# Performance work log

Hardware: AMD Instinct MI355X
Metric: run time of the kernel (lower is better)

The kernel has to match this reference:

```python
import jax, jax.numpy as jnp
import numpy as np


def gcn_conv(x, edge_index, W, b):
    """PyG-style GCNConv: add self-loops, symmetric D^-1/2 (A+I) D^-1/2 norm,
    linear transform before propagation, bias after aggregation."""
    N = x.shape[0]
    src, dst = edge_index[0], edge_index[1]
    loops = jnp.arange(N, dtype=edge_index.dtype)
    src_a = jnp.concatenate([src, loops])  # [E+N]
    dst_a = jnp.concatenate([dst, loops])
    deg = jax.ops.segment_sum(jnp.ones_like(src_a, dtype=x.dtype), dst_a, num_segments=N)
    inv_sqrt = jnp.where(deg > 0, jax.lax.rsqrt(deg), 0.0)
    norm = inv_sqrt[src_a] * inv_sqrt[dst_a]  # [E+N]
    h = x @ W  # [N, out]
    out = jax.ops.segment_sum(h[src_a] * norm[:, None], dst_a, num_segments=N)
    return out + b


def gcn_branch(x, edge_index, W1, b1, W2, b2):
    h = jax.nn.relu(gcn_conv(x, edge_index, W1, b1))
    h = jax.nn.relu(gcn_conv(h, edge_index, W2, b2))
    # global_add_pool with batch = zeros -> sum over all nodes, shape [1, h2]
    return jnp.sum(h, axis=0, keepdims=True)


def setup_inputs() -> dict:
    key = jax.random.key(0)
    ks = jax.random.split(key, 12)
    Nm, Em = 50000, 800000
    Np, Ep = 100000, 1600000
    h1, h2 = 128, 128
    fc_in = 2 * h2 + 1
    inp = {
        "mol_x": jax.random.normal(ks[0], (Nm, 1), jnp.float32),
        "mol_edge_index": jax.random.randint(ks[1], (2, Em), 0, Nm, jnp.int64),
        "prot_x": jax.random.normal(ks[2], (Np, 1), jnp.float32),
        "prot_edge_index": jax.random.randint(ks[3], (2, Ep), 0, Np, jnp.int64),
        "phys_energy": jax.random.normal(ks[4], (1,), jnp.float32),
        "W1": jax.random.normal(ks[5], (1, h1), jnp.float32) / np.sqrt(1.0),
        "b1": jnp.zeros((h1,), jnp.float32),
        "W2": jax.random.normal(ks[6], (h1, h2), jnp.float32) / np.sqrt(h1),
        "b2": jnp.zeros((h2,), jnp.float32),
        "Wfc": jax.random.normal(ks[7], (fc_in, 1), jnp.float32) / np.sqrt(fc_in),
        "bfc": jnp.zeros((1,), jnp.float32),
    }
    return inp


def reference(mol_x, mol_edge_index, prot_x, prot_edge_index, phys_energy,
              W1, b1, W2, b2, Wfc, bfc):
    x1 = gcn_branch(mol_x, mol_edge_index, W1, b1, W2, b2)    # [1, h2]
    x2 = gcn_branch(prot_x, prot_edge_index, W1, b1, W2, b2)  # [1, h2]
    combined = jnp.concatenate([x1, x2, phys_energy.reshape(1, -1)], axis=-1)
    return combined @ Wfc + bfc  # [1, 1]
```

## Files before the change

### kernel.cpp

```cpp
#include <hip/hip_runtime.h>

#define CDIV(a,b) (((a)+(b)-1)/(b))
#define BINCAP 4096


__global__ __launch_bounds__(256) void k_count(
        const int* __restrict__ me, const int* __restrict__ pe,
        int Em, int Ep, int Nm, int per, int NBKT, int* __restrict__ btot,
        const float* __restrict__ b1, const float* __restrict__ W1,
        const float* __restrict__ W2, float* __restrict__ u, float* __restrict__ v,
        int* __restrict__ flags) {
    __shared__ int cnt[64];
    __shared__ int nz;
    int t = threadIdx.x, blk = blockIdx.x;
    int Etot = Em + Ep;
    int e0 = blk * per, e1 = min(e0 + per, Etot);
    if (t < 64) cnt[t] = 0;
    __syncthreads();
    for (int e = e0 + t; e < e1; e += 256) {
        int d = (e < Em) ? me[Em + e] : (pe[Ep + (e - Em)] + Nm);
        atomicAdd(&cnt[d >> 12], 1);
    }
    __syncthreads();
    if (t < NBKT && cnt[t]) atomicAdd(&btot[t], cnt[t]);
    if (blk == 0) {
        if (t == 0) nz = 0;
        __syncthreads();
        if (t < 128) {
            if (b1[t] != 0.f) atomicOr(&nz, 1);
            float au = 0.f, av = 0.f;
            for (int j = 0; j < 128; ++j) {
                float w = W1[j], w2 = W2[j * 128 + t];
                au = fmaf(fmaxf(w, 0.f), w2, au);
                av = fmaf(fmaxf(-w, 0.f), w2, av);
            }
            u[t] = au; v[t] = av;
        }
        __syncthreads();
        if (t == 0) flags[0] = nz;
    }
}

__global__ __launch_bounds__(256) void k_bin(
        const int* __restrict__ me, const int* __restrict__ pe,
        int Em, int Ep, int Nm, int per, int NBKT,
        const int* __restrict__ btot, int* __restrict__ gcur, int* __restrict__ pkb) {
    __shared__ int lpk[BINCAP];
    __shared__ unsigned char lbkt[BINCAP];
    __shared__ int cnt[64], cst[64], cur[64], wbase[64], bb[64];
    int t = threadIdx.x;
    int Etot = Em + Ep;
    int e0 = blockIdx.x * per, e1 = min(e0 + per, Etot);
    int ne = max(e1 - e0, 0);
    if (t < 64) cnt[t] = 0;
    __syncthreads();
    for (int e = e0 + t; e < e1; e += 256) {
        int d = (e < Em) ? me[Em + e] : (pe[Ep + (e - Em)] + Nm);
        atomicAdd(&cnt[d >> 12], 1);
    }
    __syncthreads();
    if (t == 0) {
        int run = 0, runb = 0;
        for (int b = 0; b < NBKT; ++b) {
            cst[b] = run; cur[b] = run; run += cnt[b];
            bb[b] = runb; runb += btot[b];
        }
    }
    __syncthreads();
    if (t < NBKT) wbase[t] = bb[t] + (cnt[t] ? atomicAdd(&gcur[t], cnt[t]) : 0);
    __syncthreads();
    for (int e = e0 + t; e < e1; e += 256) {
        int s, d;
        if (e < Em) { s = me[e];            d = me[Em + e]; }
        else        { int ee = e - Em; s = pe[ee] + Nm; d = pe[Ep + ee] + Nm; }
        int b = d >> 12;
        int p = atomicAdd(&cur[b], 1);
        lpk[p]  = ((d & 4095) << 18) | s;
        lbkt[p] = (unsigned char)b;
    }
    __syncthreads();
    for (int i = t; i < ne; i += 256) {
        int b = lbkt[i];
        pkb[wbase[b] + (i - cst[b])] = lpk[i];
    }
}

__global__ __launch_bounds__(256) void k_accA(
        const int* __restrict__ pkb, const int* __restrict__ btot,
        int NBKT, int WPB, int Ntot, int* __restrict__ hist) {
    __shared__ int h[4096];
    __shared__ int sbs, sbe;
    int b = blockIdx.x / WPB, sl = blockIdx.x % WPB, t = threadIdx.x;
    if (t == 0) {
        int run = 0;
        for (int i = 0; i < b; ++i) run += btot[i];
        sbs = run; sbe = run + btot[b];
    }
    for (int k = t; k < 4096; k += 256) h[k] = 0;
    __syncthreads();
    for (int i = sbs + sl * 256 + t; i < sbe; i += WPB * 256)
        atomicAdd(&h[pkb[i] >> 18], 1);
    __syncthreads();
    for (int k = t; k < 4096; k += 256) {
        int vv = h[k];
        int node = (b << 12) + k;
        if (vv && node < Ntot) atomicAdd(&hist[node], vv);
    }
}

__global__ void k_inv(const int* __restrict__ hist,
                      const float* __restrict__ mx, const float* __restrict__ px,
                      int Nm, int Ntot, float* __restrict__ xi) {
    int g = blockIdx.x * 256 + threadIdx.x;
    if (g < Ntot) {
        float x = (g < Nm) ? mx[g] : px[g - Nm];
        xi[g] = x * rsqrtf((float)(hist[g] + 1));
    }
}

__global__ __launch_bounds__(256) void k_accB(
        const int* __restrict__ pkb, const int* __restrict__ btot,
        const float* __restrict__ xi, int NBKT, int WPB, int Ntot,
        float* __restrict__ s_acc) {
    __shared__ float acc[4096];
    __shared__ int sbs, sbe;
    int b = blockIdx.x / WPB, sl = blockIdx.x % WPB, t = threadIdx.x;
    if (t == 0) {
        int run = 0;
        for (int i = 0; i < b; ++i) run += btot[i];
        sbs = run; sbe = run + btot[b];
    }
    for (int k = t; k < 4096; k += 256) acc[k] = 0.f;
    __syncthreads();
    for (int i = sbs + sl * 256 + t; i < sbe; i += WPB * 256) {
        int pk = pkb[i];
        atomicAdd(&acc[pk >> 18], xi[pk & 0x3FFFF]);
    }
    __syncthreads();
    for (int k = t; k < 4096; k += 256) {
        float vv = acc[k];
        int node = (b << 12) + k;
        if (vv != 0.f && node < Ntot) atomicAdd(&s_acc[node], vv);
    }
}

__global__ void k_s(const int* __restrict__ hist, const float* __restrict__ s_acc,
                    const float* __restrict__ xi, int Ntot, float2* __restrict__ si) {
    int i = blockIdx.x * 256 + threadIdx.x;
    if (i >= Ntot) return;
    float iv = rsqrtf((float)(hist[i] + 1));
    si[i] = make_float2(iv * (s_acc[i] + xi[i]), iv);
}

__global__ __launch_bounds__(256) void k_accC(
        const int* __restrict__ pkb, const int* __restrict__ btot,
        const float2* __restrict__ si, int NBKT, int WPB, int Ntot,
        float* __restrict__ PM, const int* __restrict__ flags) {
    if (flags[0]) return;
    __shared__ float pm[8192];
    __shared__ int sbs, sbe;
    int b = blockIdx.x / WPB, sl = blockIdx.x % WPB, t = threadIdx.x;
    if (t == 0) {
        int run = 0;
        for (int i = 0; i < b; ++i) run += btot[i];
        sbs = run; sbe = run + btot[b];
    }
    for (int k = t; k < 8192; k += 256) pm[k] = 0.f;
    __syncthreads();
    for (int i = sbs + sl * 256 + t; i < sbe; i += WPB * 256) {
        int pk = pkb[i];
        float2 q = si[pk & 0x3FFFF];
        float val = q.y * q.x;
        int lo = (pk >> 18) * 2;
        if (val > 0.f)      atomicAdd(&pm[lo],     val);
        else if (val < 0.f) atomicAdd(&pm[lo + 1], -val);
    }
    __syncthreads();
    for (int k = t; k < 8192; k += 256) {
        float vv = pm[k];
        int node = (b << 12) + (k >> 1);
        if (vv != 0.f && node < Ntot) atomicAdd(&PM[2 * node + (k & 1)], vv);
    }
}

__global__ __launch_bounds__(256) void k_pool_fact(
        const float2* __restrict__ si, const float* __restrict__ PM,
        const float* __restrict__ u, const float* __restrict__ v,
        const float* __restrict__ b2, int Nm, int Np, int gm, int gp,
        float* __restrict__ pool, const int* __restrict__ flags) {
    if (flags[0]) return;
    __shared__ float sA[2][128], sB[2][128], sR[2][128];
    int t = threadIdx.x;
    int k = t & 127;
    int grp = t >> 7;
    int blk = blockIdx.x;
    int base, cnt, gstart, gsize;
    float* poolOut;
    if (blk < gm) { base = 0;  cnt = Nm; gstart = blk;      gsize = gm; poolOut = pool; }
    else          { base = Nm; cnt = Np; gstart = blk - gm; gsize = gp; poolOut = pool + 128; }
    float uk = u[k], vk = v[k], bk = b2[k];
    float acc = 0.f;
    int ntile = (cnt + 127) >> 7;
    for (int tb = gstart * 2; tb < ntile; tb += gsize * 2) {
        int tile = tb + grp;
        int d0 = base + tile * 128;
        int nn = (tile < ntile) ? min(128, base + cnt - d0) : 0;
        float A = 0.f, B = 0.f;
        if (k < nn) {
            float2 q  = si[d0 + k];
            float2 pm = *(const float2*)&PM[2 * (d0 + k)];
            float iv = q.y;
            A = iv * fmaf(iv, fmaxf(q.x, 0.f), pm.x);
            B = iv * fmaf(iv, fmaxf(-q.x, 0.f), pm.y);
        }
        __syncthreads();
        sA[grp][k] = A;
        sB[grp][k] = B;
        __syncthreads();
        #pragma unroll 8
        for (int i = 0; i < nn; ++i)
            acc += fmaxf(fmaf(sA[grp][i], uk, fmaf(sB[grp][i], vk, bk)), 0.f);
    }
    __syncthreads();
    sR[grp][k] = acc;
    __syncthreads();
    if (t < 128) atomicAdd(&poolOut[t], sR[0][t] + sR[1][t]);
}

__global__ void k_final(const float* __restrict__ pool, const float* __restrict__ phys,
                        const float* __restrict__ Wfc, const float* __restrict__ bfc,
                        float* __restrict__ out) {
    __shared__ float sm[256];
    int t = threadIdx.x;
    float acc = pool[t] * Wfc[t];
    if (t == 0) acc += phys[0] * Wfc[256] + bfc[0];
    sm[t] = acc;
    __syncthreads();
    for (int off = 128; off > 0; off >>= 1) {
        if (t < off) sm[t] += sm[t + off];
        __syncthreads();
    }
    if (t == 0) out[0] = sm[0];
}

__global__ __launch_bounds__(1024) void k_fallback(
        const int* __restrict__ me, const int* __restrict__ pe,
        int Em, int Ep, int Nm, int Np,
        const int* __restrict__ hist, const float2* __restrict__ si,
        const float* __restrict__ W1, const float* __restrict__ b1,
        const float* __restrict__ W2, const float* __restrict__ b2,
        const float* __restrict__ phys, const float* __restrict__ Wfc,
        const float* __restrict__ bfc,
        int* __restrict__ rowst, int* __restrict__ cursor, int* __restrict__ sorted,
        float* __restrict__ pool, float* __restrict__ out,
        const int* __restrict__ flags) {
    if (!flags[0]) return;
    int t = threadIdx.x;
    int Ntot = Nm + Np, Etot = Em + Ep;
    __shared__ int ipart[1024];
    __shared__ float wrow[16][128];
    __shared__ float fred[256];
    int per = CDIV(Ntot, 1024);
    int a0 = min(t * per, Ntot), a1 = min(a0 + per, Ntot);
    int ssum = 0;
    for (int i = a0; i < a1; ++i) ssum += hist[i];
    ipart[t] = ssum;
    __syncthreads();
    if (t == 0) {
        int run = 0;
        for (int i = 0; i < 1024; ++i) { int vv = ipart[i]; ipart[i] = run; run += vv; }
    }
    __syncthreads();
    int run = ipart[t];
    for (int i = a0; i < a1; ++i) { rowst[i] = run; cursor[i] = run; run += hist[i]; }
    __threadfence();
    __syncthreads();
    for (int e = t; e < Etot; e += 1024) {
        int s, d;
        if (e < Em) { s = me[e];            d = me[Em + e]; }
        else        { int ee = e - Em; s = pe[ee] + Nm; d = pe[Ep + ee] + Nm; }
        int p = atomicAdd(&cursor[d], 1);
        sorted[p] = s;
    }
    __threadfence();
    __syncthreads();
    int wid = t >> 6, lane = t & 63;
    float wa = W1[lane], wb = W1[lane + 64], ba = b1[lane], bb2 = b1[lane + 64];
    float pMa = 0.f, pMb = 0.f, pPa = 0.f, pPb = 0.f;
    for (int d = wid; d < Ntot; d += 16) {
        int st = rowst[d], en = st + hist[d];
        float aa = 0.f, ab = 0.f;
        for (int e = st; e < en; ++e) {
            float2 q = si[sorted[e]];
            aa = fmaf(q.y, fmaxf(fmaf(q.x, wa, ba ), 0.f), aa);
            ab = fmaf(q.y, fmaxf(fmaf(q.x, wb, bb2), 0.f), ab);
        }
        float2 ps = si[d];
        float oa = fmaxf(fmaf(ps.x, wa, ba ), 0.f);
        float ob = fmaxf(fmaf(ps.x, wb, bb2), 0.f);
        aa = ps.y * (aa + ps.y * oa);
        ab = ps.y * (ab + ps.y * ob);
        wrow[wid][lane]      = aa;
        wrow[wid][lane + 64] = ab;
        float acc0 = b2[lane], acc1 = b2[lane + 64];
        for (int j = 0; j < 128; ++j) {
            float aj = wrow[wid][j];
            acc0 = fmaf(aj, W2[j * 128 + lane],      acc0);
            acc1 = fmaf(aj, W2[j * 128 + lane + 64], acc1);
        }
        float r0 = fmaxf(acc0, 0.f), r1 = fmaxf(acc1, 0.f);
        if (d < Nm) { pMa += r0; pMb += r1; } else { pPa += r0; pPb += r1; }
    }
    atomicAdd(&pool[lane],            pMa);
    atomicAdd(&pool[lane + 64],       pMb);
    atomicAdd(&pool[128 + lane],      pPa);
    atomicAdd(&pool[128 + lane + 64], pPb);
    __threadfence();
    __syncthreads();
    if (t < 256) fred[t] = atomicAdd(&pool[t], 0.f) * Wfc[t];
    __syncthreads();
    for (int off = 128; off > 0; off >>= 1) {
        if (t < off) fred[t] += fred[t + off];
        __syncthreads();
    }
    if (t == 0) out[0] = fred[0] + phys[0] * Wfc[256] + bfc[0];
}

extern "C" void kernel_launch(void* const* d_in, const int* in_sizes, int n_in,
                              void* d_out, int out_size, void* d_ws, size_t ws_size,
                              hipStream_t stream) {
    const float* mol_x  = (const float*)d_in[0];
    const int*   mol_e  = (const int*)  d_in[1];
    const float* prot_x = (const float*)d_in[2];
    const int*   prot_e = (const int*)  d_in[3];
    const float* phys   = (const float*)d_in[4];
    const float* W1     = (const float*)d_in[5];
    const float* b1     = (const float*)d_in[6];
    const float* W2     = (const float*)d_in[7];
    const float* b2     = (const float*)d_in[8];
    const float* Wfc    = (const float*)d_in[9];
    const float* bfc    = (const float*)d_in[10];
    float* out = (float*)d_out;

    int Nm = in_sizes[0], Em = in_sizes[1] / 2;
    int Np = in_sizes[2], Ep = in_sizes[3] / 2;
    int Ntot = Nm + Np, Etot = Em + Ep;

    int NBKT = CDIV(Ntot, 4096);
    int NBIN = CDIV(Etot, BINCAP);
    int per  = CDIV(Etot, NBIN);

    char* p = (char*)d_ws;
    auto alloc = [&](size_t bytes) -> char* {
        char* r = p;
        p += (bytes + 255) & ~(size_t)255;
        return r;
    };
    int*    sorted= (int*)   alloc((size_t)Etot * 4);
    int*    pkb   = (int*)   alloc((size_t)Etot * 4);
    int*    hist  = (int*)   alloc((size_t)Ntot * 4);
    float*  s_acc = (float*) alloc((size_t)Ntot * 4);
    float*  PM    = (float*) alloc((size_t)Ntot * 8);
    float*  pool  = (float*) alloc(256 * 4);
    int*    btot  = (int*)   alloc(64 * 4);
    int*    gcur  = (int*)   alloc(64 * 4);
    int*    rowst = (int*)   alloc((size_t)Ntot * 4);
    int*    cursor= (int*)   alloc((size_t)Ntot * 4);
    float*  xi    = (float*) alloc((size_t)Ntot * 4);
    float2* si    = (float2*)alloc((size_t)Ntot * 8);
    float*  u     = (float*) alloc(128 * 4);
    float*  v     = (float*) alloc(128 * 4);
    int*    flags = (int*)   alloc(256);

    size_t zbytes = (char*)(gcur + 64) - (char*)hist;
    hipMemsetAsync(hist, 0, zbytes, stream);

    int B = CDIV(Ntot, 256);
    const int WPB_A = 32, WPB_B = 32, WPB_C = 16;

    k_count<<<NBIN, 256, 0, stream>>>(mol_e, prot_e, Em, Ep, Nm, per, NBKT, btot,
                                      b1, W1, W2, u, v, flags);
    k_bin  <<<NBIN, 256, 0, stream>>>(mol_e, prot_e, Em, Ep, Nm, per, NBKT,
                                      btot, gcur, pkb);
    k_accA <<<NBKT * WPB_A, 256, 0, stream>>>(pkb, btot, NBKT, WPB_A, Ntot, hist);
    k_inv  <<<B, 256, 0, stream>>>(hist, mol_x, prot_x, Nm, Ntot, xi);
    k_accB <<<NBKT * WPB_B, 256, 0, stream>>>(pkb, btot, xi, NBKT, WPB_B, Ntot, s_acc);
    k_s    <<<B, 256, 0, stream>>>(hist, s_acc, xi, Ntot, si);
    k_accC <<<NBKT * WPB_C, 256, 0, stream>>>(pkb, btot, si, NBKT, WPB_C, Ntot,
                                              PM, flags);
    {
        int gm = CDIV(CDIV(Nm, 128), 2);
        int gp = CDIV(CDIV(Np, 128), 2);
        k_pool_fact<<<gm + gp, 256, 0, stream>>>(si, PM, u, v, b2, Nm, Np, gm, gp,
                                                 pool, flags);
    }
    k_final<<<1, 256, 0, stream>>>(pool, phys, Wfc, bfc, out);
    k_fallback<<<1, 1024, 0, stream>>>(mol_e, prot_e, Em, Ep, Nm, Np, hist, si,
                                       W1, b1, W2, b2, phys, Wfc, bfc,
                                       rowst, cursor, sorted, pool, out, flags);
}
```

Measured before the change: 159.4 us.

## Replace global two-pass binning with per-chunk local sort and bucket directory

Merges the count and bin kernels into one pass: each 4096-edge chunk sorts its edges by destination bucket in shared memory and writes them back contiguously, along with a per-chunk bucket offset directory. The accumulation kernels then walk every chunk's slice for their bucket instead of a globally contiguous bucket range. This removes one edge-read pass, the global atomics and the scattered writes. In exchange, the consumers read short, fragmented segments and do extra directory lookups. It also folds the final FC kernel into the fallback kernel and lowers WPB_A from 32 to 16.

```diff
diff --git a/kernel.cpp b/kernel.cpp
--- a/kernel.cpp
+++ b/kernel.cpp
@@ -1,20 +1,23 @@
 #include <hip/hip_runtime.h>
 
 #define CDIV(a,b) (((a)+(b)-1)/(b))
-#define BINCAP 4096
-
-
-__global__ __launch_bounds__(256) void k_count(
+#define CHUNK 4096
+
+
+__global__ __launch_bounds__(256) void k_bin2(
         const int* __restrict__ me, const int* __restrict__ pe,
-        int Em, int Ep, int Nm, int per, int NBKT, int* __restrict__ btot,
+        int Em, int Ep, int Nm, int NBKT,
+        int* __restrict__ pkb, int* __restrict__ cdir,
         const float* __restrict__ b1, const float* __restrict__ W1,
         const float* __restrict__ W2, float* __restrict__ u, float* __restrict__ v,
         int* __restrict__ flags) {
-    __shared__ int cnt[64];
+    __shared__ int lpk[CHUNK];
+    __shared__ int cnt[64], cst[65], cur[64];
     __shared__ int nz;
-    int t = threadIdx.x, blk = blockIdx.x;
+    int t = threadIdx.x, c = blockIdx.x;
     int Etot = Em + Ep;
-    int e0 = blk * per, e1 = min(e0 + per, Etot);
+    int e0 = c * CHUNK, e1 = min(e0 + CHUNK, Etot);
+    int ne = e1 - e0;
     if (t < 64) cnt[t] = 0;
     __syncthreads();
     for (int e = e0 + t; e < e1; e += 256) {
@@ -22,8 +25,24 @@
         atomicAdd(&cnt[d >> 12], 1);
     }
     __syncthreads();
-    if (t < NBKT && cnt[t]) atomicAdd(&btot[t], cnt[t]);
-    if (blk == 0) {
+    if (t == 0) {
+        int run = 0;
+        for (int b = 0; b < NBKT; ++b) { cst[b] = run; cur[b] = run; run += cnt[b]; }
+        cst[NBKT] = run;
+    }
+    __syncthreads();
+    for (int e = e0 + t; e < e1; e += 256) {
+        int s, d;
+        if (e < Em) { s = me[e];            d = me[Em + e]; }
+        else        { int ee = e - Em; s = pe[ee] + Nm; d = pe[Ep + ee] + Nm; }
+        int b = d >> 12;
+        int p = atomicAdd(&cur[b], 1);
+        lpk[p] = ((d & 4095) << 18) | s;
+    }
+    __syncthreads();
+    if (t <= NBKT) cdir[c * (NBKT + 1) + t] = cst[t];
+    for (int i = t; i < ne; i += 256) pkb[e0 + i] = lpk[i];
+    if (c == 0) {
         if (t == 0) nz = 0;
         __syncthreads();
         if (t < 128) {
@@ -41,69 +60,25 @@
     }
 }
 
-__global__ __launch_bounds__(256) void k_bin(
-        const int* __restrict__ me, const int* __restrict__ pe,
-        int Em, int Ep, int Nm, int per, int NBKT,
-        const int* __restrict__ btot, int* __restrict__ gcur, int* __restrict__ pkb) {
-    __shared__ int lpk[BINCAP];
-    __shared__ unsigned char lbkt[BINCAP];
-    __shared__ int cnt[64], cst[64], cur[64], wbase[64], bb[64];
-    int t = threadIdx.x;
-    int Etot = Em + Ep;
-    int e0 = blockIdx.x * per, e1 = min(e0 + per, Etot);
-    int ne = max(e1 - e0, 0);
-    if (t < 64) cnt[t] = 0;
-    __syncthreads();
-    for (int e = e0 + t; e < e1; e += 256) {
-        int d = (e < Em) ? me[Em + e] : (pe[Ep + (e - Em)] + Nm);
-        atomicAdd(&cnt[d >> 12], 1);
-    }
-    __syncthreads();
-    if (t == 0) {
-        int run = 0, runb = 0;
-        for (int b = 0; b < NBKT; ++b) {
-            cst[b] = run; cur[b] = run; run += cnt[b];
-            bb[b] = runb; runb += btot[b];
-        }
-    }
-    __syncthreads();
-    if (t < NBKT) wbase[t] = bb[t] + (cnt[t] ? atomicAdd(&gcur[t], cnt[t]) : 0);
-    __syncthreads();
-    for (int e = e0 + t; e < e1; e += 256) {
-        int s, d;
-        if (e < Em) { s = me[e];            d = me[Em + e]; }
-        else        { int ee = e - Em; s = pe[ee] + Nm; d = pe[Ep + ee] + Nm; }
-        int b = d >> 12;
-        int p = atomicAdd(&cur[b], 1);
-        lpk[p]  = ((d & 4095) << 18) | s;
-        lbkt[p] = (unsigned char)b;
-    }
-    __syncthreads();
-    for (int i = t; i < ne; i += 256) {
-        int b = lbkt[i];
-        pkb[wbase[b] + (i - cst[b])] = lpk[i];
-    }
-}
-
 __global__ __launch_bounds__(256) void k_accA(
-        const int* __restrict__ pkb, const int* __restrict__ btot,
-        int NBKT, int WPB, int Ntot, int* __restrict__ hist) {
+        const int* __restrict__ pkb, const int* __restrict__ cdir,
+        int NBIN, int NBKT, int WPB, int Ntot, int* __restrict__ hist) {
     __shared__ int h[4096];
-    __shared__ int sbs, sbe;
     int b = blockIdx.x / WPB, sl = blockIdx.x % WPB, t = threadIdx.x;
-    if (t == 0) {
-        int run = 0;
-        for (int i = 0; i < b; ++i) run += btot[i];
-        sbs = run; sbe = run + btot[b];
-    }
     for (int k = t; k < 4096; k += 256) h[k] = 0;
     __syncthreads();
-    for (int i = sbs + sl * 256 + t; i < sbe; i += WPB * 256)
-        atomicAdd(&h[pkb[i] >> 18], 1);
-    __syncthreads();
+    for (int c = sl; c < NBIN; c += WPB) {
+        int base = c * (NBKT + 1);
+        int s0 = cdir[base + b], s1 = cdir[base + b + 1];
+        int p0 = c << 12;
+        for (int i = s0 + t; i < s1; i += 256)
+            atomicAdd(&h[pkb[p0 + i] >> 18], 1);
+    }
+    __syncthreads();
+    int nb = b << 12;
     for (int k = t; k < 4096; k += 256) {
         int vv = h[k];
-        int node = (b << 12) + k;
+        int node = nb + k;
         if (vv && node < Ntot) atomicAdd(&hist[node], vv);
     }
 }
@@ -119,27 +94,27 @@
 }
 
 __global__ __launch_bounds__(256) void k_accB(
-        const int* __restrict__ pkb, const int* __restrict__ btot,
-        const float* __restrict__ xi, int NBKT, int WPB, int Ntot,
+        const int* __restrict__ pkb, const int* __restrict__ cdir,
+        const float* __restrict__ xi, int NBIN, int NBKT, int WPB, int Ntot,
         float* __restrict__ s_acc) {
     __shared__ float acc[4096];
-    __shared__ int sbs, sbe;
     int b = blockIdx.x / WPB, sl = blockIdx.x % WPB, t = threadIdx.x;
-    if (t == 0) {
-        int run = 0;
-        for (int i = 0; i < b; ++i) run += btot[i];
-        sbs = run; sbe = run + btot[b];
-    }
     for (int k = t; k < 4096; k += 256) acc[k] = 0.f;
     __syncthreads();
-    for (int i = sbs + sl * 256 + t; i < sbe; i += WPB * 256) {
-        int pk = pkb[i];
-        atomicAdd(&acc[pk >> 18], xi[pk & 0x3FFFF]);
-    }
-    __syncthreads();
+    for (int c = sl; c < NBIN; c += WPB) {
+        int base = c * (NBKT + 1);
+        int s0 = cdir[base + b], s1 = cdir[base + b + 1];
+        int p0 = c << 12;
+        for (int i = s0 + t; i < s1; i += 256) {
+            int pk = pkb[p0 + i];
+            atomicAdd(&acc[pk >> 18], xi[pk & 0x3FFFF]);
+        }
+    }
+    __syncthreads();
+    int nb = b << 12;
     for (int k = t; k < 4096; k += 256) {
         float vv = acc[k];
-        int node = (b << 12) + k;
+        int node = nb + k;
         if (vv != 0.f && node < Ntot) atomicAdd(&s_acc[node], vv);
     }
 }
@@ -153,32 +128,32 @@
 }
 
 __global__ __launch_bounds__(256) void k_accC(
-        const int* __restrict__ pkb, const int* __restrict__ btot,
-        const float2* __restrict__ si, int NBKT, int WPB, int Ntot,
+        const int* __restrict__ pkb, const int* __restrict__ cdir,
+        const float2* __restrict__ si, int NBIN, int NBKT, int WPB, int Ntot,
         float* __restrict__ PM, const int* __restrict__ flags) {
     if (flags[0]) return;
     __shared__ float pm[8192];
-    __shared__ int sbs, sbe;
     int b = blockIdx.x / WPB, sl = blockIdx.x % WPB, t = threadIdx.x;
-    if (t == 0) {
-        int run = 0;
-        for (int i = 0; i < b; ++i) run += btot[i];
-        sbs = run; sbe = run + btot[b];
-    }
     for (int k = t; k < 8192; k += 256) pm[k] = 0.f;
     __syncthreads();
-    for (int i = sbs + sl * 256 + t; i < sbe; i += WPB * 256) {
-        int pk = pkb[i];
-        float2 q = si[pk & 0x3FFFF];
-        float val = q.y * q.x;
-        int lo = (pk >> 18) * 2;
-        if (val > 0.f)      atomicAdd(&pm[lo],     val);
-        else if (val < 0.f) atomicAdd(&pm[lo + 1], -val);
-    }
-    __syncthreads();
+    for (int c = sl; c < NBIN; c += WPB) {
+        int base = c * (NBKT + 1);
+        int s0 = cdir[base + b], s1 = cdir[base + b + 1];
+        int p0 = c << 12;
+        for (int i = s0 + t; i < s1; i += 256) {
+            int pk = pkb[p0 + i];
+            float2 q = si[pk & 0x3FFFF];
+            float val = q.y * q.x;
+            int lo = (pk >> 18) * 2;
+            if (val > 0.f)      atomicAdd(&pm[lo],     val);
+            else if (val < 0.f) atomicAdd(&pm[lo + 1], -val);
+        }
+    }
+    __syncthreads();
+    int nb = b << 12;
     for (int k = t; k < 8192; k += 256) {
         float vv = pm[k];
-        int node = (b << 12) + (k >> 1);
+        int node = nb + (k >> 1);
         if (vv != 0.f && node < Ntot) atomicAdd(&PM[2 * node + (k & 1)], vv);
     }
 }
@@ -227,23 +202,7 @@
     if (t < 128) atomicAdd(&poolOut[t], sR[0][t] + sR[1][t]);
 }
 
-__global__ void k_final(const float* __restrict__ pool, const float* __restrict__ phys,
-                        const float* __restrict__ Wfc, const float* __restrict__ bfc,
-                        float* __restrict__ out) {
-    __shared__ float sm[256];
-    int t = threadIdx.x;
-    float acc = pool[t] * Wfc[t];
-    if (t == 0) acc += phys[0] * Wfc[256] + bfc[0];
-    sm[t] = acc;
-    __syncthreads();
-    for (int off = 128; off > 0; off >>= 1) {
-        if (t < off) sm[t] += sm[t + off];
-        __syncthreads();
-    }
-    if (t == 0) out[0] = sm[0];
-}
-
-__global__ __launch_bounds__(1024) void k_fallback(
+__global__ __launch_bounds__(1024) void k_tail(
         const int* __restrict__ me, const int* __restrict__ pe,
         int Em, int Ep, int Nm, int Np,
         const int* __restrict__ hist, const float2* __restrict__ si,
@@ -254,8 +213,22 @@
         int* __restrict__ rowst, int* __restrict__ cursor, int* __restrict__ sorted,
         float* __restrict__ pool, float* __restrict__ out,
         const int* __restrict__ flags) {
-    if (!flags[0]) return;
     int t = threadIdx.x;
+    if (flags[0] == 0) {
+        __shared__ float sm[256];
+        if (t < 256) {
+            float acc = pool[t] * Wfc[t];
+            if (t == 0) acc += phys[0] * Wfc[256] + bfc[0];
+            sm[t] = acc;
+        }
+        __syncthreads();
+        for (int off = 128; off > 0; off >>= 1) {
+            if (t < off) sm[t] += sm[t + off];
+            __syncthreads();
+        }
+        if (t == 0) out[0] = sm[0];
+        return;
+    }
     int Ntot = Nm + Np, Etot = Em + Ep;
     __shared__ int ipart[1024];
     __shared__ float wrow[16][128];
@@ -347,8 +320,7 @@
     int Ntot = Nm + Np, Etot = Em + Ep;
 
     int NBKT = CDIV(Ntot, 4096);
-    int NBIN = CDIV(Etot, BINCAP);
-    int per  = CDIV(Etot, NBIN);
+    int NBIN = CDIV(Etot, CHUNK);
 
     char* p = (char*)d_ws;
     auto alloc = [&](size_t bytes) -> char* {
@@ -357,13 +329,12 @@
         return r;
     };
     int*    sorted= (int*)   alloc((size_t)Etot * 4);
-    int*    pkb   = (int*)   alloc((size_t)Etot * 4);
+    int*    pkb   = (int*)   alloc((size_t)NBIN * CHUNK * 4);
+    int*    cdir  = (int*)   alloc((size_t)NBIN * (NBKT + 1) * 4);
     int*    hist  = (int*)   alloc((size_t)Ntot * 4);
     float*  s_acc = (float*) alloc((size_t)Ntot * 4);
     float*  PM    = (float*) alloc((size_t)Ntot * 8);
     float*  pool  = (float*) alloc(256 * 4);
-    int*    btot  = (int*)   alloc(64 * 4);
-    int*    gcur  = (int*)   alloc(64 * 4);
     int*    rowst = (int*)   alloc((size_t)Ntot * 4);
     int*    cursor= (int*)   alloc((size_t)Ntot * 4);
     float*  xi    = (float*) alloc((size_t)Ntot * 4);
@@ -372,30 +343,28 @@
     float*  v     = (float*) alloc(128 * 4);
     int*    flags = (int*)   alloc(256);
 
-    size_t zbytes = (char*)(gcur + 64) - (char*)hist;
+    size_t zbytes = (char*)(pool + 256) - (char*)hist;
     hipMemsetAsync(hist, 0, zbytes, stream);
 
     int B = CDIV(Ntot, 256);
-    const int WPB_A = 32, WPB_B = 32, WPB_C = 16;
-
-    k_count<<<NBIN, 256, 0, stream>>>(mol_e, prot_e, Em, Ep, Nm, per, NBKT, btot,
-                                      b1, W1, W2, u, v, flags);
-    k_bin  <<<NBIN, 256, 0, stream>>>(mol_e, prot_e, Em, Ep, Nm, per, NBKT,
-                                      btot, gcur, pkb);
-    k_accA <<<NBKT * WPB_A, 256, 0, stream>>>(pkb, btot, NBKT, WPB_A, Ntot, hist);
-    k_inv  <<<B, 256, 0, stream>>>(hist, mol_x, prot_x, Nm, Ntot, xi);
-    k_accB <<<NBKT * WPB_B, 256, 0, stream>>>(pkb, btot, xi, NBKT, WPB_B, Ntot, s_acc);
-    k_s    <<<B, 256, 0, stream>>>(hist, s_acc, xi, Ntot, si);
-    k_accC <<<NBKT * WPB_C, 256, 0, stream>>>(pkb, btot, si, NBKT, WPB_C, Ntot,
-                                              PM, flags);
+    const int WPB_A = 16, WPB_B = 32, WPB_C = 16;
+
+    k_bin2<<<NBIN, 256, 0, stream>>>(mol_e, prot_e, Em, Ep, Nm, NBKT, pkb, cdir,
+                                     b1, W1, W2, u, v, flags);
+    k_accA<<<NBKT * WPB_A, 256, 0, stream>>>(pkb, cdir, NBIN, NBKT, WPB_A, Ntot, hist);
+    k_inv <<<B, 256, 0, stream>>>(hist, mol_x, prot_x, Nm, Ntot, xi);
+    k_accB<<<NBKT * WPB_B, 256, 0, stream>>>(pkb, cdir, xi, NBIN, NBKT, WPB_B, Ntot,
+                                             s_acc);
+    k_s   <<<B, 256, 0, stream>>>(hist, s_acc, xi, Ntot, si);
+    k_accC<<<NBKT * WPB_C, 256, 0, stream>>>(pkb, cdir, si, NBIN, NBKT, WPB_C, Ntot,
+                                             PM, flags);
     {
         int gm = CDIV(CDIV(Nm, 128), 2);
         int gp = CDIV(CDIV(Np, 128), 2);
         k_pool_fact<<<gm + gp, 256, 0, stream>>>(si, PM, u, v, b2, Nm, Np, gm, gp,
                                                  pool, flags);
     }
-    k_final<<<1, 256, 0, stream>>>(pool, phys, Wfc, bfc, out);
-    k_fallback<<<1, 1024, 0, stream>>>(mol_e, prot_e, Em, Ep, Nm, Np, hist, si,
-                                       W1, b1, W2, b2, phys, Wfc, bfc,
-                                       rowst, cursor, sorted, pool, out, flags);
-}
+    k_tail<<<1, 1024, 0, stream>>>(mol_e, prot_e, Em, Ep, Nm, Np, hist, si,
+                                   W1, b1, W2, b2, phys, Wfc, bfc,
+                                   rowst, cursor, sorted, pool, out, flags);
+}
```

Measured after the change: 133.2 us. 16.4% less time.
